# Optimization experiments

Hardware: AMD Instinct MI355X
Metric: run time of the kernel (lower is better)

Reference implementation:

```python
import jax, jax.numpy as jnp
import numpy as np

B, S, E = 32, 128, 128
NQ, NS = 100000, 512
QN, SN = 4, 10
S_MAX = 4
NEG = -1e30


def setup_inputs() -> dict:
    key = jax.random.key(0)
    ks = jax.random.split(key, 24)
    def nrm(k, shape, sc):
        return jax.random.normal(k, shape, jnp.float32) * sc
    inp = {}
    inp['question'] = jax.random.randint(ks[0], (B, S), 0, NQ, jnp.int32)
    inp['response'] = jax.random.randint(ks[1], (B, S), 0, 2, jnp.int32)
    inp['mask'] = jax.random.randint(ks[2], (B, S), 0, 2, jnp.int32)
    inp['q_neighbors'] = jax.random.randint(ks[3], (NQ, QN), 0, NS, jnp.int32)
    inp['s_neighbors'] = jax.random.randint(ks[4], (NS, SN), 0, NQ, jnp.int32)
    sidx = jax.random.randint(ks[5], (NQ, S_MAX), 0, NS, jnp.int32)
    inp['qs_table'] = jnp.zeros((NQ, NS), jnp.float32).at[jnp.arange(NQ)[:, None], sidx].set(1.0)
    inp['emb_q'] = nrm(ks[6], (NQ, E), 1.0)
    inp['emb_s'] = nrm(ks[7], (NS, E), 1.0)
    inp['emb_r'] = nrm(ks[8], (2, E), 1.0)
    s_in = 1.0 / np.sqrt(2 * E).astype(np.float32)
    s_e = 1.0 / np.sqrt(E).astype(np.float32)
    inp['W_ih'] = nrm(ks[9], (4 * E, 2 * E), s_in)
    inp['b_ih'] = nrm(ks[10], (4 * E,), s_in)
    inp['b_hh'] = nrm(ks[11], (4 * E,), s_in)
    inp['W_agg'] = nrm(ks[12], (3, E, E), s_e)
    inp['b_agg'] = nrm(ks[13], (3, E), s_e)
    inp['W_last'] = nrm(ks[14], (E, E), s_e)
    inp['b_last'] = nrm(ks[15], (E,), s_e)
    inp['W_query'] = nrm(ks[16], (E, E), s_e)
    inp['b_query'] = nrm(ks[17], (E,), s_e)
    inp['W_key'] = nrm(ks[18], (E, E), s_e)
    inp['b_key'] = nrm(ks[19], (E,), s_e)
    inp['w_W'] = nrm(ks[20], (2 * E,), s_in)
    inp['b_W'] = nrm(ks[21], (), s_in)
    return inp


def _forward(question, response, mask, q_neighbors, s_neighbors, qs_table,
             emb_q, emb_s, emb_r, W_ih, b_ih, b_hh, W_agg, b_agg, W_last, b_last,
             W_query, b_query, W_key, b_key, w_W, b_W):
    Bq, Sq = question.shape
    Ed = emb_q.shape[1]
    AGG = W_agg.shape[0]
    w_q, w_k = w_W[:Ed], w_W[Ed:]
    c_pad = jnp.tanh(b_query) @ w_k  # attention logit piece of an all-zero padded state
    pos = jnp.arange(Sq)

    def step(state_history, xs):
        t, q_t, r_t, m_t, q_next = xs
        # ---- multi-hop neighbor gather (q -> s -> q -> s) ----
        n1 = q_neighbors[q_t]              # [B,QN] skill ids
        n2 = s_neighbors[n1]               # [B,QN,SN] question ids
        n3 = q_neighbors[n2]               # [B,QN,SN,QN] skill ids
        e = [emb_q[q_t], emb_s[n1], emb_q[n2], emb_s[n3]]
        # triangular mean-aggregate (dropout is identity in eval mode)
        for i in range(AGG):
            for j in range(AGG - i):
                e[j] = jnp.tanh((e[j + 1].mean(-2) + e[j]) @ W_agg[j].T + b_agg[j])
        agg = jnp.tanh(e[0] @ W_last.T + b_last)
        emb_qt = jnp.where((m_t == 1)[:, None], agg, emb_q[q_t])
        # ---- LSTMCell with zero initial (h, c): W_hh @ 0 drops out, b_hh remains ----
        x = jnp.concatenate([emb_qt, emb_r[r_t]], -1)
        gates = x @ W_ih.T + b_ih + b_hh
        gi, gf, gg, go = jnp.split(gates, 4, -1)
        h = jax.nn.sigmoid(go) * jnp.tanh(jax.nn.sigmoid(gi) * jnp.tanh(gg))
        # ---- skills related to next question; zero-padded rows contribute exactly 0 ----
        vals, sidx = jax.lax.top_k(qs_table[q_next], S_MAX)
        emb_sk = emb_s[sidx] * (vals > 0.0)[..., None]
        qs_concat = jnp.concatenate([emb_q[q_next][:, None], emb_sk], 1)  # [B,1+S_MAX,E]
        # ---- hard recap: history steps whose question is a 2-hop neighbor of q_next ----
        q_rel = s_neighbors[q_neighbors[q_next]].reshape(Bq, -1)          # [B,QN*SN]
        matches = (question[:, :, None] == q_rel[:, None, :]).any(-1) & (pos[None, :] < t)
        n_sel = matches.sum(-1)
        P = (jnp.max(n_sel) - n_sel).astype(jnp.float32)  # zero-pad count to per-batch max
        # ---- predict: MLP_W(concat(Q,K)) is rank-1 => logit = a[b,q] + c[b,s] ----
        a = jnp.tanh(qs_concat @ W_key.T + b_key) @ w_q + b_W             # [B,Qd]
        c_hist = jnp.tanh(state_history @ W_query.T + b_query) @ w_k      # [B,S]
        c_cur = jnp.tanh(h @ W_query.T + b_query) @ w_k                   # [B]
        lh = jnp.where(matches[:, None, :], a[:, :, None] + c_hist[:, None, :], NEG)
        lc = a + c_cur[:, None]
        lp = a + c_pad
        m = jnp.maximum(jnp.maximum(lh.max(-1), lc), lp)
        Eh = jnp.exp(lh - m[:, :, None])
        Ec = jnp.exp(lc - m)
        Ep = jnp.exp(lp - m)
        g_hist = jnp.einsum('bqe,bse->bqs', qs_concat, state_history)
        g_cur = jnp.einsum('bqe,be->bq', qs_concat, h)
        denom = Eh.sum(-1) + Ec + P[:, None] * Ep  # zero-pad states counted analytically
        num = (Eh * g_hist).sum(-1) + Ec * g_cur   # pads multiply g=0 -> no numerator term
        y = jax.nn.sigmoid(jnp.sum(num / denom, axis=1))
        # original skips the state write at t == 0 (slot 0 stays zero forever)
        state_history = state_history.at[:, t].set(jnp.where(t > 0, h, jnp.zeros_like(h)))
        return state_history, y

    ts = jnp.arange(Sq - 1)
    xs = (ts, question[:, :-1].T, response[:, :-1].T, mask[:, :-1].T, question[:, 1:].T)
    init = jnp.zeros((Bq, Sq, Ed), jnp.float32)
    _, ys = jax.lax.scan(step, init, xs)
    return jnp.zeros((Bq, Sq), jnp.float32).at[:, 0].set(0.5).at[:, 1:].set(ys.T)


def reference(question, response, mask, q_neighbors, s_neighbors, qs_table,
              emb_q, emb_s, emb_r, W_ih, b_ih, b_hh, W_agg, b_agg, W_last, b_last,
              W_query, b_query, W_key, b_key, w_W, b_W):
    return _forward(question, response, mask, q_neighbors, s_neighbors, qs_table,
                    emb_q, emb_s, emb_r, W_ih, b_ih, b_hh, W_agg, b_agg, W_last, b_last,
                    W_query, b_query, W_key, b_key, w_W, b_W)
```

## Files before the change

### kernel.cpp

```cpp
#include <hip/hip_runtime.h>
#include <stdint.h>

#define NB 32
#define SEQ 128
#define EMB 128
#define NSTEP 127
#define NS 512

__device__ __forceinline__ float ftanh(float x){ float e=__expf(2.f*x); return 1.f-2.f/(e+1.f); }
__device__ __forceinline__ float fsig(float x){ return 1.f/(1.f+__expf(-x)); }
__device__ __forceinline__ float4 ld4(const float* p){ return *(const float4*)p; }

#define FMA4(acc, xv, a0, a1, a2, a3) \
  acc.x = fmaf(xv.x, a0.x, fmaf(xv.y, a1.x, fmaf(xv.z, a2.x, fmaf(xv.w, a3.x, acc.x)))); \
  acc.y = fmaf(xv.x, a0.y, fmaf(xv.y, a1.y, fmaf(xv.z, a2.y, fmaf(xv.w, a3.y, acc.y)))); \
  acc.z = fmaf(xv.x, a0.z, fmaf(xv.y, a1.z, fmaf(xv.z, a2.z, fmaf(xv.w, a3.z, acc.z)))); \
  acc.w = fmaf(xv.x, a0.w, fmaf(xv.y, a1.w, fmaf(xv.z, a2.w, fmaf(xv.w, a3.w, acc.w))));

template<int K, int XS>
__device__ __forceinline__ void gemmKS(const float* __restrict__ WT, int NEtot,
                                       const float* Xl, const float* __restrict__ bias,
                                       float* outb, float* partb)
{
  const int tid = threadIdx.x;
  const int et = tid & 31;
  const int kt = (tid >> 5) & 1;
  const int rg = tid >> 6;
  constexpr int KH = K/2;
  constexpr int G  = KH/4;
  const float* wp = WT + (size_t)kt*KH*NEtot + et*4;
  const float* xr = Xl + (size_t)(rg*2)*XS + kt*KH;
  float4 a0 = {0.f,0.f,0.f,0.f};
  float4 a1 = {0.f,0.f,0.f,0.f};
  float4 w0 = ld4(wp);
  float4 w1 = ld4(wp + NEtot);
  float4 w2 = ld4(wp + 2*NEtot);
  float4 w3 = ld4(wp + 3*NEtot);
  const float* wq = wp + (size_t)4*NEtot;
  float4 m0 = ld4(wq);
  float4 m1 = ld4(wq + NEtot);
  float4 m2 = ld4(wq + 2*NEtot);
  float4 m3 = ld4(wq + 3*NEtot);
  #pragma unroll 2
  for (int g = 0; g + 2 < G; g += 2) {
    const float* wa = wp + (size_t)(4*(g+2))*NEtot;
    float4 n0 = ld4(wa);
    float4 n1 = ld4(wa + NEtot);
    float4 n2 = ld4(wa + 2*NEtot);
    float4 n3 = ld4(wa + 3*NEtot);
    float4 xa0 = ld4(xr + 4*g);
    float4 xa1 = ld4(xr + XS + 4*g);
    FMA4(a0, xa0, w0, w1, w2, w3);
    FMA4(a1, xa1, w0, w1, w2, w3);
    w0=n0; w1=n1; w2=n2; w3=n3;
    const float* wb = wp + (size_t)(4*(g+3))*NEtot;
    float4 o0 = ld4(wb);
    float4 o1 = ld4(wb + NEtot);
    float4 o2 = ld4(wb + 2*NEtot);
    float4 o3 = ld4(wb + 3*NEtot);
    float4 xb0 = ld4(xr + 4*(g+1));
    float4 xb1 = ld4(xr + XS + 4*(g+1));
    FMA4(a0, xb0, m0, m1, m2, m3);
    FMA4(a1, xb1, m0, m1, m2, m3);
    m0=o0; m1=o1; m2=o2; m3=o3;
  }
  {
    float4 xa0 = ld4(xr + 4*(G-2));
    float4 xa1 = ld4(xr + XS + 4*(G-2));
    FMA4(a0, xa0, w0, w1, w2, w3);
    FMA4(a1, xa1, w0, w1, w2, w3);
    float4 xb0 = ld4(xr + 4*(G-1));
    float4 xb1 = ld4(xr + XS + 4*(G-1));
    FMA4(a0, xb0, m0, m1, m2, m3);
    FMA4(a1, xb1, m0, m1, m2, m3);
  }
  float* dst;
  if (kt == 0) {
    float4 bb = ld4(bias + et*4);
    a0.x+=bb.x; a0.y+=bb.y; a0.z+=bb.z; a0.w+=bb.w;
    a1.x+=bb.x; a1.y+=bb.y; a1.z+=bb.z; a1.w+=bb.w;
    dst = outb;
  } else {
    dst = partb;
  }
  float* ob = dst + (size_t)(rg*2)*132 + et*4;
  *(float4*)(ob)       = a0;
  *(float4*)(ob + 132) = a1;
}

__global__ __launch_bounds__(256) void k_T(
    const float* __restrict__ W_agg, const float* __restrict__ W_last,
    const float* __restrict__ W_query, const float* __restrict__ W_ih,
    const float* __restrict__ b_ih, const float* __restrict__ b_hh,
    const float* __restrict__ b_query, const float* __restrict__ w_W,
    const float* __restrict__ emb_r,
    float* __restrict__ WT012, float* __restrict__ WLT, float* __restrict__ WQT,
    float* __restrict__ WIHT, float* __restrict__ ER2,
    float* __restrict__ BIH, float* __restrict__ CPAD,
    float* __restrict__ G1, int* __restrict__ Pmaxi)
{
  const int gid = blockIdx.x*256 + threadIdx.x;
  const int gsz = gridDim.x*256;
  for (int i = gid; i < 49152; i += gsz) {
    int j = i >> 14, rem = i & 16383, k = rem >> 7, e = rem & 127;
    WT012[i] = W_agg[j*16384 + e*128 + k];
  }
  for (int i = gid; i < 16384; i += gsz) {
    int k = i >> 7, e = i & 127;
    WLT[i] = W_last[e*128 + k];
    WQT[i] = W_query[e*128 + k];
  }
  for (int i = gid; i < 65536; i += gsz) {
    int k = i >> 9, e = i & 511;
    WIHT[i] = W_ih[e*256 + k];
  }
  for (int i = gid; i < 1024; i += gsz) {
    int r = i >> 9, c = i & 511;
    const float* wcol = W_ih + (size_t)c*256 + 128;
    const float* er = emb_r + r*128;
    float acc = 0.f;
    #pragma unroll 4
    for (int k = 0; k < 128; k += 4) {
      acc = fmaf(er[k], wcol[k],
            fmaf(er[k+1], wcol[k+1],
            fmaf(er[k+2], wcol[k+2],
            fmaf(er[k+3], wcol[k+3], acc))));
    }
    ER2[i] = acc;
  }
  for (int i = gid; i < 65536; i += gsz) G1[i] = 0.f;
  if (gid < 512) BIH[gid] = b_ih[gid] + b_hh[gid];
  if (gid < 128) Pmaxi[gid] = 0;
  if (blockIdx.x == 0) {
    __shared__ float red[256];
    float v = (threadIdx.x < 128) ? ftanh(b_query[threadIdx.x]) * w_W[128 + threadIdx.x] : 0.f;
    red[threadIdx.x] = v; __syncthreads();
    #pragma unroll
    for (int s = 128; s > 0; s >>= 1) {
      if (threadIdx.x < s) red[threadIdx.x] += red[threadIdx.x + s];
      __syncthreads();
    }
    if (threadIdx.x == 0) CPAD[0] = red[0];
  }
}

__global__ __launch_bounds__(512) void k_pre(
    const int* __restrict__ s_neighbors, const int* __restrict__ q_neighbors,
    const float* __restrict__ emb_q, const float* __restrict__ emb_s,
    const float* __restrict__ WT012, const float* __restrict__ b_agg,
    float* __restrict__ E1, float* __restrict__ G1)
{
  __shared__ float XA[16*132];
  __shared__ float XB[16*132];
  __shared__ float PB[16*132];
  __shared__ int idx[160];
  __shared__ int n3[64];
  const int tid = threadIdx.x;
  const int blk = blockIdx.x;
  if (blk < 32) {
    const int s0 = blk*16;
    if (tid < 160) idx[tid] = s_neighbors[s0*10 + tid];
    __syncthreads();
    {
      const int e4 = (tid & 31) << 2;
      const int rr = tid >> 5;
      float4 a = ld4(emb_s + (size_t)(s0+rr)*128 + e4);
      float sx=0,sy=0,sz=0,sw=0;
      #pragma unroll
      for (int jj = 0; jj < 10; ++jj) {
        float4 q = ld4(emb_q + (size_t)idx[rr*10+jj]*128 + e4);
        sx+=q.x; sy+=q.y; sz+=q.z; sw+=q.w;
      }
      float4 o; o.x=a.x+0.1f*sx; o.y=a.y+0.1f*sy; o.z=a.z+0.1f*sz; o.w=a.w+0.1f*sw;
      *(float4*)(XA + rr*132 + e4) = o;
    }
    __syncthreads();
    gemmKS<128,132>(WT012 + 16384, 128, XA, b_agg + 128, XB, PB);
    __syncthreads();
    for (int f = tid; f < 2048; f += 512) {
      int r = f >> 7, e = f & 127, i = r*132 + e;
      E1[(size_t)(s0+r)*128 + e] = ftanh(XB[i] + PB[i]);
    }
  } else {
    const int p0 = (blk-32)*16;
    if (tid < 16) idx[tid] = s_neighbors[p0 + tid];
    __syncthreads();
    if (tid < 64) n3[tid] = q_neighbors[(size_t)idx[tid>>2]*4 + (tid&3)];
    __syncthreads();
    {
      const int e4 = (tid & 31) << 2;
      const int rr = tid >> 5;
      float4 a = ld4(emb_q + (size_t)idx[rr]*128 + e4);
      float sx=0,sy=0,sz=0,sw=0;
      #pragma unroll
      for (int k = 0; k < 4; ++k) {
        float4 q = ld4(emb_s + (size_t)n3[rr*4+k]*128 + e4);
        sx+=q.x; sy+=q.y; sz+=q.z; sw+=q.w;
      }
      float4 o; o.x=a.x+0.25f*sx; o.y=a.y+0.25f*sy; o.z=a.z+0.25f*sz; o.w=a.w+0.25f*sw;
      *(float4*)(XA + rr*132 + e4) = o;
    }
    __syncthreads();
    gemmKS<128,132>(WT012 + 32768, 128, XA, b_agg + 256, XB, PB);
    __syncthreads();
    for (int f = tid; f < 2048; f += 512) {
      int r = f >> 7, e = f & 127, i = r*132 + e;
      atomicAdd(&G1[(size_t)((p0+r)/10)*128 + e], ftanh(XB[i] + PB[i]));
    }
  }
}

__global__ __launch_bounds__(512) void k_pre2(
    const float* __restrict__ E1, const float* __restrict__ G1,
    const float* __restrict__ WT012, const float* __restrict__ b_agg,
    float* __restrict__ E2)
{
  __shared__ float XA[16*132];
  __shared__ float XB[16*132];
  __shared__ float PB[16*132];
  const int tid = threadIdx.x;
  const int s0 = blockIdx.x*16;
  for (int f = tid; f < 2048; f += 512) {
    int r = f >> 7, e = f & 127;
    XA[r*132 + e] = 0.1f*G1[(size_t)(s0+r)*128 + e] + E1[(size_t)(s0+r)*128 + e];
  }
  __syncthreads();
  gemmKS<128,132>(WT012 + 16384, 128, XA, b_agg + 128, XB, PB);
  __syncthreads();
  for (int f = tid; f < 2048; f += 512) {
    int r = f >> 7, e = f & 127, i = r*132 + e;
    E2[(size_t)(s0+r)*128 + e] = ftanh(XB[i] + PB[i]);
  }
}

__global__ __launch_bounds__(512) void k_chain(
    const int* __restrict__ question, const int* __restrict__ response,
    const int* __restrict__ maskp, const int* __restrict__ q_neighbors,
    const int* __restrict__ s_neighbors,
    const float* __restrict__ emb_q, const float* __restrict__ emb_s,
    const float* __restrict__ WT012, const float* __restrict__ WLT,
    const float* __restrict__ WQT, const float* __restrict__ WIHT,
    const float* __restrict__ ER2, const float* __restrict__ BIH,
    const float* __restrict__ b_agg, const float* __restrict__ b_last,
    const float* __restrict__ b_query, const float* __restrict__ w_W,
    const float* __restrict__ E1, const float* __restrict__ E2,
    float* __restrict__ Hfull, float* __restrict__ Cq,
    int* __restrict__ nsel, unsigned long long* __restrict__ mwords,
    int* __restrict__ Pmaxi)
{
  __shared__ float XA[16*132];
  __shared__ float XB[16*132];
  __shared__ float M1[16*132];
  __shared__ float M2[16*132];
  __shared__ float PB[16*132];
  __shared__ float XC[16*132];
  __shared__ int qts[16], rts[16], mts[16], n1s[64];

  const int tid = threadIdx.x;
  const int blk = blockIdx.x;

  if (tid < 16) {
    int rid = blk*16 + tid;
    int b = rid / 127, t = rid - b*127;
    qts[tid] = question[b*SEQ + t];
    rts[tid] = response[b*SEQ + t];
    mts[tid] = maskp[b*SEQ + t];
  }
  __syncthreads();
  if (tid < 64) n1s[tid] = q_neighbors[(size_t)qts[tid>>2]*4 + (tid&3)];
  __syncthreads();
  {
    const int e4 = (tid & 31) << 2;
    const int rr = tid >> 5;
    const int* nn = n1s + rr*4;
    float4 a = ld4(emb_q + (size_t)qts[rr]*128 + e4);
    float s1x=0,s1y=0,s1z=0,s1w=0, s2x=0,s2y=0,s2z=0,s2w=0, s3x=0,s3y=0,s3z=0,s3w=0;
    #pragma unroll
    for (int i = 0; i < 4; ++i) {
      float4 q1 = ld4(emb_s + (size_t)nn[i]*128 + e4);
      float4 q2 = ld4(E1 + (size_t)nn[i]*128 + e4);
      float4 q3 = ld4(E2 + (size_t)nn[i]*128 + e4);
      s1x+=q1.x; s1y+=q1.y; s1z+=q1.z; s1w+=q1.w;
      s2x+=q2.x; s2y+=q2.y; s2z+=q2.z; s2w+=q2.w;
      s3x+=q3.x; s3y+=q3.y; s3z+=q3.z; s3w+=q3.w;
    }
    float4 o; o.x=a.x+0.25f*s1x; o.y=a.y+0.25f*s1y; o.z=a.z+0.25f*s1z; o.w=a.w+0.25f*s1w;
    *(float4*)(XA + rr*132 + e4) = o;
    float4 p; p.x=0.25f*s2x; p.y=0.25f*s2y; p.z=0.25f*s2z; p.w=0.25f*s2w;
    *(float4*)(M1 + rr*132 + e4) = p;
    float4 u; u.x=0.25f*s3x; u.y=0.25f*s3y; u.z=0.25f*s3z; u.w=0.25f*s3w;
    *(float4*)(M2 + rr*132 + e4) = u;
  }
  __syncthreads();
  gemmKS<128,132>(WT012, 128, XA, b_agg, XB, PB);
  __syncthreads();
  for (int f = tid; f < 2048; f += 512) {
    int i = (f >> 7)*132 + (f & 127);
    XB[i] = M1[i] + ftanh(XB[i] + PB[i]);
  }
  __syncthreads();
  gemmKS<128,132>(WT012, 128, XB, b_agg, XA, PB);
  __syncthreads();
  for (int f = tid; f < 2048; f += 512) {
    int i = (f >> 7)*132 + (f & 127);
    XA[i] = M2[i] + ftanh(XA[i] + PB[i]);
  }
  __syncthreads();
  gemmKS<128,132>(WT012, 128, XA, b_agg, XB, PB);
  __syncthreads();
  for (int f = tid; f < 2048; f += 512) {
    int i = (f >> 7)*132 + (f & 127);
    XB[i] = ftanh(XB[i] + PB[i]);
  }
  __syncthreads();
  gemmKS<128,132>(WLT, 128, XB, b_last, XA, PB);
  __syncthreads();
  for (int f = tid; f < 2048; f += 512) {
    int r = f >> 7, e = f & 127, i = r*132 + e;
    float agg = ftanh(XA[i] + PB[i]);
    XC[i] = (mts[r] == 1) ? agg : emb_q[(size_t)qts[r]*128 + e];
  }
  __syncthreads();
  gemmKS<128,132>(WIHT,       512, XC, BIH,       XA, PB);
  __syncthreads();
  for (int f = tid; f < 2048; f += 512) {
    int r = f >> 7, e = f & 127, i = r*132 + e;
    XA[i] += PB[i] + ER2[rts[r]*512 + e];
  }
  __syncthreads();
  gemmKS<128,132>(WIHT + 256, 512, XC, BIH + 256, XB, PB);
  __syncthreads();
  for (int f = tid; f < 2048; f += 512) {
    int r = f >> 7, e = f & 127, i = r*132 + e;
    XB[i] += PB[i] + ER2[rts[r]*512 + 256 + e];
  }
  __syncthreads();
  gemmKS<128,132>(WIHT + 384, 512, XC, BIH + 384, M1, PB);
  __syncthreads();
  for (int f = tid; f < 2048; f += 512) {
    int r = f >> 7, e = f & 127, i = r*132 + e;
    float gi = XA[i], gg = XB[i];
    float go = M1[i] + PB[i] + ER2[rts[r]*512 + 384 + e];
    float h = fsig(go) * ftanh(fsig(gi) * ftanh(gg));
    XC[i] = h;
    Hfull[(size_t)(blk*16 + r)*128 + e] = h;
  }
  __syncthreads();
  gemmKS<128,132>(WQT, 128, XC, b_query, XA, PB);
  __syncthreads();
  {
    const int et = tid & 31, rr = tid >> 5;
    float4 wv = ld4(w_W + 128 + et*4);
    float4 o = ld4(XA + rr*132 + et*4);
    float4 p = ld4(PB + rr*132 + et*4);
    float s = ftanh(o.x+p.x)*wv.x + ftanh(o.y+p.y)*wv.y
            + ftanh(o.z+p.z)*wv.z + ftanh(o.w+p.w)*wv.w;
    #pragma unroll
    for (int off = 16; off > 0; off >>= 1) s += __shfl_down(s, off);
    if (et == 0) Cq[blk*16 + rr] = s;
  }
  {
    const int wv = tid >> 6;
    const int ln = tid & 63;
    for (int rr = wv; rr < 16; rr += 8) {
      int rid = blk*16 + rr;
      int b = rid / 127, t = rid - b*127;
      int q_next = question[b*SEQ + t + 1];
      int qrv = 0;
      if (ln < 40)
        qrv = s_neighbors[(size_t)q_neighbors[(size_t)q_next*4 + ln/10]*10 + ln%10];
      int q0 = question[b*SEQ + ln];
      int q1 = question[b*SEQ + 64 + ln];
      bool p0 = false, p1 = false;
      #pragma unroll 8
      for (int i = 0; i < 40; ++i) {
        int qv = __shfl(qrv, i);
        p0 |= (q0 == qv); p1 |= (q1 == qv);
      }
      p0 &= (ln < t);
      p1 &= (64 + ln < t);
      unsigned long long w0 = __ballot(p0);
      unsigned long long w1 = __ballot(p1);
      if (ln == 0) {
        size_t bt = (size_t)b*NSTEP + t;
        mwords[bt*2 + 0] = w0;
        mwords[bt*2 + 1] = w1;
        int ns = __popcll(w0) + __popcll(w1);
        nsel[bt] = ns;
        atomicMax(&Pmaxi[t], ns);
      }
    }
  }
}

__device__ __forceinline__ float xsum(float v) {
  #pragma unroll
  for (int o = 32; o > 0; o >>= 1) v += __shfl_xor(v, o);
  return v;
}
__device__ __forceinline__ float xmax(float v) {
  #pragma unroll
  for (int o = 32; o > 0; o >>= 1) v = fmaxf(v, __shfl_xor(v, o));
  return v;
}

__global__ __launch_bounds__(512) void k_attn(
    const int* __restrict__ question, const float* __restrict__ qs_table,
    const float* __restrict__ emb_q, const float* __restrict__ emb_s,
    const float* __restrict__ CPAD,
    const float* __restrict__ Hfull, const float* __restrict__ Cq,
    const int* __restrict__ nsel, const unsigned long long* __restrict__ mwords,
    const int* __restrict__ Pmaxi, float* __restrict__ out)
{
  __shared__ float us[8][128];
  const int tid = threadIdx.x;
  const int wv = tid >> 6;
  const int ln = tid & 63;
  const int pid = blockIdx.x*8 + wv;
  const int b = pid / NSTEP, t = pid - b*NSTEP;
  const size_t bt = (size_t)b*NSTEP + t;
  const int q_next = question[b*SEQ + t + 1];

  float4 v0 = ld4(qs_table + (size_t)q_next*NS + ln*4);
  float4 v1 = ld4(qs_table + (size_t)q_next*NS + 256 + ln*4);
  unsigned long long m0b = __ballot(v0.x > 0.f);
  unsigned long long m1b = __ballot(v0.y > 0.f);
  unsigned long long m2b = __ballot(v0.z > 0.f);
  unsigned long long m3b = __ballot(v0.w > 0.f);
  unsigned long long m4b = __ballot(v1.x > 0.f);
  unsigned long long m5b = __ballot(v1.y > 0.f);
  unsigned long long m6b = __ballot(v1.z > 0.f);
  unsigned long long m7b = __ballot(v1.w > 0.f);

  float ue0 = emb_q[(size_t)q_next*EMB + ln];
  float ue1 = emb_q[(size_t)q_next*EMB + 64 + ln];
  {
    int added = 0;
    unsigned long long mm[1];
    #define SCAN(MB, KOFF, BASE) \
      { unsigned long long m = MB; \
        while (m && added < 4) { \
          int i = __ffsll((unsigned long long)m) - 1; m &= m - 1ull; \
          int c = BASE + i*4 + KOFF; \
          ue0 += emb_s[(size_t)c*EMB + ln]; \
          ue1 += emb_s[(size_t)c*EMB + 64 + ln]; \
          ++added; } }
    SCAN(m0b, 0, 0) SCAN(m1b, 1, 0) SCAN(m2b, 2, 0) SCAN(m3b, 3, 0)
    SCAN(m4b, 0, 256) SCAN(m5b, 1, 256) SCAN(m6b, 2, 256) SCAN(m7b, 3, 256)
    #undef SCAN
    (void)mm;
  }
  us[wv][ln] = ue0;
  us[wv][64 + ln] = ue1;

  const float c_pad = CPAD[0];
  const float P = (float)(Pmaxi[t] - nsel[bt]);
  const float c_cur = Cq[bt];
  const unsigned long long w0 = mwords[bt*2 + 0];
  const unsigned long long w1 = mwords[bt*2 + 1];

  float gcp = ue0*Hfull[bt*EMB + ln] + ue1*Hfull[bt*EMB + 64 + ln];
  float gc = xsum(gcp);

  float M, Sexp = 0.f, Snum = 0.f;
  if ((w0 | w1) == 0ull) {
    M = fmaxf(c_cur, c_pad);
  } else {
    const bool ma = (w0 >> ln) & 1ull;
    const bool mb = (w1 >> ln) & 1ull;
    float Cp0 = ma ? ((ln == 0) ? c_pad : Cq[(size_t)b*NSTEP + ln]) : -3.0e38f;
    float Cp1 = mb ? Cq[(size_t)b*NSTEP + 64 + ln] : -3.0e38f;
    float mh = xmax(fmaxf(Cp0, Cp1));
    M = fmaxf(mh, fmaxf(c_cur, c_pad));
    float wgt0 = ma ? __expf(Cp0 - M) : 0.f;
    float wgt1 = mb ? __expf(Cp1 - M) : 0.f;
    __threadfence_block();
    float d0 = 0.f, d1 = 0.f;
    if (ma && ln >= 1) {
      const float* hp = Hfull + ((size_t)b*NSTEP + ln)*EMB;
      const float* uu = us[wv];
      float s = 0.f;
      #pragma unroll 8
      for (int e = 0; e < 128; e += 4) {
        float4 h4 = ld4(hp + e);
        s = fmaf(uu[e],h4.x, fmaf(uu[e+1],h4.y, fmaf(uu[e+2],h4.z, fmaf(uu[e+3],h4.w, s))));
      }
      d0 = s;
    }
    if (mb) {
      const float* hp = Hfull + ((size_t)b*NSTEP + 64 + ln)*EMB;
      const float* uu = us[wv];
      float s = 0.f;
      #pragma unroll 8
      for (int e = 0; e < 128; e += 4) {
        float4 h4 = ld4(hp + e);
        s = fmaf(uu[e],h4.x, fmaf(uu[e+1],h4.y, fmaf(uu[e+2],h4.z, fmaf(uu[e+3],h4.w, s))));
      }
      d1 = s;
    }
    Sexp = xsum(wgt0 + wgt1);
    Snum = xsum(fmaf(wgt0, d0, wgt1 * d1));
  }
  if (ln == 0) {
    float Ec = __expf(c_cur - M), Ep = __expf(c_pad - M);
    float D = Sexp + Ec + P * Ep;
    float numt = Snum + Ec * gc;
    out[b*SEQ + t + 1] = fsig(numt / D);
    if (t == 0) out[b*SEQ] = 0.5f;
  }
}

extern "C" void kernel_launch(void* const* d_in, const int* in_sizes, int n_in,
                              void* d_out, int out_size, void* d_ws, size_t ws_size,
                              hipStream_t stream) {
  const int* question    = (const int*)d_in[0];
  const int* response    = (const int*)d_in[1];
  const int* maskp       = (const int*)d_in[2];
  const int* q_neighbors = (const int*)d_in[3];
  const int* s_neighbors = (const int*)d_in[4];
  const float* qs_table  = (const float*)d_in[5];
  const float* emb_q     = (const float*)d_in[6];
  const float* emb_s     = (const float*)d_in[7];
  const float* emb_r     = (const float*)d_in[8];
  const float* W_ih      = (const float*)d_in[9];
  const float* b_ih      = (const float*)d_in[10];
  const float* b_hh      = (const float*)d_in[11];
  const float* W_agg     = (const float*)d_in[12];
  const float* b_agg     = (const float*)d_in[13];
  const float* W_last    = (const float*)d_in[14];
  const float* b_last    = (const float*)d_in[15];
  const float* W_query   = (const float*)d_in[16];
  const float* b_query   = (const float*)d_in[17];
  const float* w_W       = (const float*)d_in[20];
  float* out = (float*)d_out;

  float* ws = (float*)d_ws;
  float* WT012 = ws;
  float* WLT   = ws + 49152;
  float* WQT   = ws + 65536;
  float* WIHT  = ws + 81920;
  float* ER2   = ws + 147456;
  float* BIH   = ws + 212992;
  float* CPAD  = ws + 213504;
  float* E1    = ws + 213520;
  float* G1    = ws + 279056;
  float* E2    = ws + 344592;
  float* Hfull = ws + 410128;
  float* Cq    = ws + 930320;
  int*   Pmaxi = (int*)(ws + 934384);
  int*   nselp = (int*)(ws + 934512);
  unsigned long long* mwords =
      (unsigned long long*)(((uintptr_t)(ws + 938576) + 15) & ~(uintptr_t)15);

  k_T<<<dim3(512), dim3(256), 0, stream>>>(
      W_agg, W_last, W_query, W_ih, b_ih, b_hh, b_query, w_W, emb_r,
      WT012, WLT, WQT, WIHT, ER2, BIH, CPAD, G1, Pmaxi);
  k_pre<<<dim3(352), dim3(512), 0, stream>>>(
      s_neighbors, q_neighbors, emb_q, emb_s, WT012, b_agg, E1, G1);
  k_pre2<<<dim3(32), dim3(512), 0, stream>>>(E1, G1, WT012, b_agg, E2);
  k_chain<<<dim3(254), dim3(512), 0, stream>>>(
      question, response, maskp, q_neighbors, s_neighbors, emb_q, emb_s,
      WT012, WLT, WQT, WIHT, ER2, BIH, b_agg, b_last, b_query, w_W,
      E1, E2, Hfull, Cq, nselp, mwords, Pmaxi);
  k_attn<<<dim3(508), dim3(512), 0, stream>>>(
      question, qs_table, emb_q, emb_s, CPAD, Hfull, Cq,
      nselp, mwords, Pmaxi, out);
}
```

Measured before the change: 381.2 us.

## Fuse k_pre2 into k_pre via spin-wait counter and batch LSTM gate GEMMs

Merges the second-hop aggregation kernel into k_pre. The 320 G1-producing blocks are reordered to launch first and bump a global counter, and the 32 E-blocks spin on that counter before computing E2 in place. This removes one kernel launch and a round trip of E1 through global memory. Separately, k_chain issues its three gate GEMMs back to back into separate shared buffers (adding XD), which removes the intermediate barriers and elementwise passes. The cost is extra shared memory, which may lower occupancy, and an inter-block spin wait that depends on the producer blocks being scheduled.

```diff
diff --git a/kernel.cpp b/kernel.cpp
--- a/kernel.cpp
+++ b/kernel.cpp
@@ -97,7 +97,7 @@
     float* __restrict__ WT012, float* __restrict__ WLT, float* __restrict__ WQT,
     float* __restrict__ WIHT, float* __restrict__ ER2,
     float* __restrict__ BIH, float* __restrict__ CPAD,
-    float* __restrict__ G1, int* __restrict__ Pmaxi)
+    float* __restrict__ G1, int* __restrict__ Pmaxi, int* __restrict__ CNT)
 {
   const int gid = blockIdx.x*256 + threadIdx.x;
   const int gsz = gridDim.x*256;
@@ -131,6 +131,7 @@
   for (int i = gid; i < 65536; i += gsz) G1[i] = 0.f;
   if (gid < 512) BIH[gid] = b_ih[gid] + b_hh[gid];
   if (gid < 128) Pmaxi[gid] = 0;
+  if (gid == 0) CNT[0] = 0;
   if (blockIdx.x == 0) {
     __shared__ float red[256];
     float v = (threadIdx.x < 128) ? ftanh(b_query[threadIdx.x]) * w_W[128 + threadIdx.x] : 0.f;
@@ -148,7 +149,8 @@
     const int* __restrict__ s_neighbors, const int* __restrict__ q_neighbors,
     const float* __restrict__ emb_q, const float* __restrict__ emb_s,
     const float* __restrict__ WT012, const float* __restrict__ b_agg,
-    float* __restrict__ E1, float* __restrict__ G1)
+    float* __restrict__ E1, float* __restrict__ G1,
+    float* __restrict__ E2, int* __restrict__ CNT)
 {
   __shared__ float XA[16*132];
   __shared__ float XB[16*132];
@@ -157,8 +159,39 @@
   __shared__ int n3[64];
   const int tid = threadIdx.x;
   const int blk = blockIdx.x;
-  if (blk < 32) {
-    const int s0 = blk*16;
+  if (blk < 320) {
+    const int p0 = blk*16;
+    if (tid < 16) idx[tid] = s_neighbors[p0 + tid];
+    __syncthreads();
+    if (tid < 64) n3[tid] = q_neighbors[(size_t)idx[tid>>2]*4 + (tid&3)];
+    __syncthreads();
+    {
+      const int e4 = (tid & 31) << 2;
+      const int rr = tid >> 5;
+      float4 a = ld4(emb_q + (size_t)idx[rr]*128 + e4);
+      float sx=0,sy=0,sz=0,sw=0;
+      #pragma unroll
+      for (int k = 0; k < 4; ++k) {
+        float4 q = ld4(emb_s + (size_t)n3[rr*4+k]*128 + e4);
+        sx+=q.x; sy+=q.y; sz+=q.z; sw+=q.w;
+      }
+      float4 o; o.x=a.x+0.25f*sx; o.y=a.y+0.25f*sy; o.z=a.z+0.25f*sz; o.w=a.w+0.25f*sw;
+      *(float4*)(XA + rr*132 + e4) = o;
+    }
+    __syncthreads();
+    gemmKS<128,132>(WT012 + 32768, 128, XA, b_agg + 256, XB, PB);
+    __syncthreads();
+    for (int f = tid; f < 2048; f += 512) {
+      int r = f >> 7, e = f & 127, i = r*132 + e;
+      atomicAdd(&G1[(size_t)((p0+r)/10)*128 + e], ftanh(XB[i] + PB[i]));
+    }
+    __syncthreads();
+    if (tid == 0) {
+      __threadfence();
+      atomicAdd(CNT, 1);
+    }
+  } else {
+    const int s0 = (blk - 320)*16;
     if (tid < 160) idx[tid] = s_neighbors[s0*10 + tid];
     __syncthreads();
     {
@@ -179,57 +212,30 @@
     __syncthreads();
     for (int f = tid; f < 2048; f += 512) {
       int r = f >> 7, e = f & 127, i = r*132 + e;
-      E1[(size_t)(s0+r)*128 + e] = ftanh(XB[i] + PB[i]);
-    }
-  } else {
-    const int p0 = (blk-32)*16;
-    if (tid < 16) idx[tid] = s_neighbors[p0 + tid];
-    __syncthreads();
-    if (tid < 64) n3[tid] = q_neighbors[(size_t)idx[tid>>2]*4 + (tid&3)];
-    __syncthreads();
-    {
-      const int e4 = (tid & 31) << 2;
-      const int rr = tid >> 5;
-      float4 a = ld4(emb_q + (size_t)idx[rr]*128 + e4);
-      float sx=0,sy=0,sz=0,sw=0;
-      #pragma unroll
-      for (int k = 0; k < 4; ++k) {
-        float4 q = ld4(emb_s + (size_t)n3[rr*4+k]*128 + e4);
-        sx+=q.x; sy+=q.y; sz+=q.z; sw+=q.w;
-      }
-      float4 o; o.x=a.x+0.25f*sx; o.y=a.y+0.25f*sy; o.z=a.z+0.25f*sz; o.w=a.w+0.25f*sw;
-      *(float4*)(XA + rr*132 + e4) = o;
-    }
-    __syncthreads();
-    gemmKS<128,132>(WT012 + 32768, 128, XA, b_agg + 256, XB, PB);
-    __syncthreads();
+      float e1 = ftanh(XB[i] + PB[i]);
+      E1[(size_t)(s0+r)*128 + e] = e1;
+      XA[i] = e1;
+    }
+    if (tid == 0) {
+      while (__hip_atomic_load(CNT, __ATOMIC_RELAXED, __HIP_MEMORY_SCOPE_AGENT) < 320) {
+        __builtin_amdgcn_s_sleep(8);
+      }
+    }
+    __syncthreads();
+    __threadfence();
     for (int f = tid; f < 2048; f += 512) {
       int r = f >> 7, e = f & 127, i = r*132 + e;
-      atomicAdd(&G1[(size_t)((p0+r)/10)*128 + e], ftanh(XB[i] + PB[i]));
-    }
-  }
-}
-
-__global__ __launch_bounds__(512) void k_pre2(
-    const float* __restrict__ E1, const float* __restrict__ G1,
-    const float* __restrict__ WT012, const float* __restrict__ b_agg,
-    float* __restrict__ E2)
-{
-  __shared__ float XA[16*132];
-  __shared__ float XB[16*132];
-  __shared__ float PB[16*132];
-  const int tid = threadIdx.x;
-  const int s0 = blockIdx.x*16;
-  for (int f = tid; f < 2048; f += 512) {
-    int r = f >> 7, e = f & 127;
-    XA[r*132 + e] = 0.1f*G1[(size_t)(s0+r)*128 + e] + E1[(size_t)(s0+r)*128 + e];
-  }
-  __syncthreads();
-  gemmKS<128,132>(WT012 + 16384, 128, XA, b_agg + 128, XB, PB);
-  __syncthreads();
-  for (int f = tid; f < 2048; f += 512) {
-    int r = f >> 7, e = f & 127, i = r*132 + e;
-    E2[(size_t)(s0+r)*128 + e] = ftanh(XB[i] + PB[i]);
+      float g1 = __hip_atomic_load(&G1[(size_t)(s0+r)*128 + e],
+                                   __ATOMIC_RELAXED, __HIP_MEMORY_SCOPE_AGENT);
+      XB[i] = 0.1f*g1 + XA[i];
+    }
+    __syncthreads();
+    gemmKS<128,132>(WT012 + 16384, 128, XB, b_agg + 128, XA, PB);
+    __syncthreads();
+    for (int f = tid; f < 2048; f += 512) {
+      int r = f >> 7, e = f & 127, i = r*132 + e;
+      E2[(size_t)(s0+r)*128 + e] = ftanh(XA[i] + PB[i]);
+    }
   }
 }
 
@@ -254,6 +260,7 @@
   __shared__ float M2[16*132];
   __shared__ float PB[16*132];
   __shared__ float XC[16*132];
+  __shared__ float XD[16*132];
   __shared__ int qts[16], rts[16], mts[16], n1s[64];
 
   const int tid = threadIdx.x;
@@ -322,25 +329,14 @@
   }
   __syncthreads();
   gemmKS<128,132>(WIHT,       512, XC, BIH,       XA, PB);
+  gemmKS<128,132>(WIHT + 256, 512, XC, BIH + 256, XB, M2);
+  gemmKS<128,132>(WIHT + 384, 512, XC, BIH + 384, M1, XD);
   __syncthreads();
   for (int f = tid; f < 2048; f += 512) {
     int r = f >> 7, e = f & 127, i = r*132 + e;
-    XA[i] += PB[i] + ER2[rts[r]*512 + e];
-  }
-  __syncthreads();
-  gemmKS<128,132>(WIHT + 256, 512, XC, BIH + 256, XB, PB);
-  __syncthreads();
-  for (int f = tid; f < 2048; f += 512) {
-    int r = f >> 7, e = f & 127, i = r*132 + e;
-    XB[i] += PB[i] + ER2[rts[r]*512 + 256 + e];
-  }
-  __syncthreads();
-  gemmKS<128,132>(WIHT + 384, 512, XC, BIH + 384, M1, PB);
-  __syncthreads();
-  for (int f = tid; f < 2048; f += 512) {
-    int r = f >> 7, e = f & 127, i = r*132 + e;
-    float gi = XA[i], gg = XB[i];
-    float go = M1[i] + PB[i] + ER2[rts[r]*512 + 384 + e];
+    float gi = XA[i] + PB[i] + ER2[rts[r]*512 + e];
+    float gg = XB[i] + M2[i] + ER2[rts[r]*512 + 256 + e];
+    float go = M1[i] + XD[i] + ER2[rts[r]*512 + 384 + e];
     float h = fsig(go) * ftanh(fsig(gi) * ftanh(gg));
     XC[i] = h;
     Hfull[(size_t)(blk*16 + r)*128 + e] = h;
@@ -436,7 +432,6 @@
   float ue1 = emb_q[(size_t)q_next*EMB + 64 + ln];
   {
     int added = 0;
-    unsigned long long mm[1];
     #define SCAN(MB, KOFF, BASE) \
       { unsigned long long m = MB; \
         while (m && added < 4) { \
@@ -448,7 +443,6 @@
     SCAN(m0b, 0, 0) SCAN(m1b, 1, 0) SCAN(m2b, 2, 0) SCAN(m3b, 3, 0)
     SCAN(m4b, 0, 256) SCAN(m5b, 1, 256) SCAN(m6b, 2, 256) SCAN(m7b, 3, 256)
     #undef SCAN
-    (void)mm;
   }
   us[wv][ln] = ue0;
   us[wv][64 + ln] = ue1;
@@ -551,13 +545,13 @@
   int*   nselp = (int*)(ws + 934512);
   unsigned long long* mwords =
       (unsigned long long*)(((uintptr_t)(ws + 938576) + 15) & ~(uintptr_t)15);
+  int*   CNT   = (int*)(mwords + 8128);
 
   k_T<<<dim3(512), dim3(256), 0, stream>>>(
       W_agg, W_last, W_query, W_ih, b_ih, b_hh, b_query, w_W, emb_r,
-      WT012, WLT, WQT, WIHT, ER2, BIH, CPAD, G1, Pmaxi);
+      WT012, WLT, WQT, WIHT, ER2, BIH, CPAD, G1, Pmaxi, CNT);
   k_pre<<<dim3(352), dim3(512), 0, stream>>>(
-      s_neighbors, q_neighbors, emb_q, emb_s, WT012, b_agg, E1, G1);
-  k_pre2<<<dim3(32), dim3(512), 0, stream>>>(E1, G1, WT012, b_agg, E2);
+      s_neighbors, q_neighbors, emb_q, emb_s, WT012, b_agg, E1, G1, E2, CNT);
   k_chain<<<dim3(254), dim3(512), 0, stream>>>(
       question, response, maskp, q_neighbors, s_neighbors, emb_q, emb_s,
       WT012, WLT, WQT, WIHT, ER2, BIH, b_agg, b_last, b_query, w_W,
```

After: 391.8 us. +2.8%, slower.
